# Kernel optimization log

Measured on AMD Instinct MI355X. Metric: run time of the kernel, lower is better.

## Reference

```python
import jax, jax.numpy as jnp
import numpy as np

NUM_HEADS = 8
SCALE_BASE = 512.0
GN_EPS = 1e-5


def rotate_every_two(x):
    x1 = x[..., ::2]
    x2 = x[..., 1::2]
    return jnp.stack([-x2, x1], axis=-1).reshape(x.shape)


def xpos_apply(x, downscale):
    # x: [B, T, D]; XPOS rotary with length-dependent scale (offset=0)
    L, D = x.shape[1], x.shape[2]
    half = D // 2
    scale_vec = (jnp.arange(0, D, 2, dtype=jnp.float32) + 0.4 * D) / (1.4 * D)  # [half]
    pos = jnp.arange(L, dtype=jnp.float32)
    scale = scale_vec[None, :] ** (pos[:, None] / SCALE_BASE)  # [L, half]
    inv_freq = 1.0 / (10000.0 ** (jnp.arange(half, dtype=jnp.float32) / half))
    sinusoid = pos[:, None] * inv_freq[None, :]  # [L, half]
    sin, cos = jnp.sin(sinusoid), jnp.cos(sinusoid)
    if downscale:
        scale = 1.0 / scale
    sin_s = jnp.repeat(sin * scale, 2, axis=-1)  # duplicate_interleave -> [L, D]
    cos_s = jnp.repeat(cos * scale, 2, axis=-1)
    return x * cos_s + rotate_every_two(x) * sin_s


def decay_mask_fn(T, num_heads):
    # gamma per head; decay stored as log(gamma) so mask = gamma^(i-j) on lower triangle
    s, e = np.log(1.0 / 32.0), np.log(1.0 / 512.0)
    gamma = 1.0 - jnp.exp(jnp.linspace(s, e, num_heads).astype(jnp.float32))
    log_decay = jnp.log(gamma)  # [H], negative
    idx = jnp.arange(T)
    expo = (idx[:, None] - idx[None, :]).astype(jnp.float32)  # i - j
    tri = (idx[:, None] >= idx[None, :])
    expo_safe = jnp.where(tri, expo, 0.0)
    mask = jnp.exp(log_decay[:, None, None] * expo_safe) * tri  # [H, T, T]
    scale = jnp.sqrt(mask.sum(axis=-1, keepdims=True))  # [H, T, 1]
    return mask / scale


def setup_inputs() -> dict:
    key = jax.random.key(0)
    ks = jax.random.split(key, 4)
    B, T, E = 2, 2048, 1024
    V = 2 * E
    return {
        "hidden_states": jax.random.normal(ks[0], (B, T, E), dtype=jnp.float32),
        "w_qkv": jax.random.normal(ks[1], (E, 2 * E + V), dtype=jnp.float32) * 0.02,
        "b_qkv": jnp.zeros((2 * E + V,), dtype=jnp.float32),
        "w_g": jax.random.normal(ks[2], (E, V), dtype=jnp.float32) * 0.02,
        "b_g": jnp.zeros((V,), dtype=jnp.float32),
        "w_p": jax.random.normal(ks[3], (V, E), dtype=jnp.float32) * 0.02,
        "b_p": jnp.zeros((E,), dtype=jnp.float32),
    }


def reference(hidden_states, w_qkv, b_qkv, w_g, b_g, w_p, b_p):
    B, T, E = hidden_states.shape
    H = NUM_HEADS
    V = 2 * E
    dk, dv = E // H, V // H

    qkv = hidden_states @ w_qkv + b_qkv
    q, k, v = qkv[..., :E], qkv[..., E:2 * E], qkv[..., 2 * E:]
    q = xpos_apply(q, downscale=False)
    k = xpos_apply(k, downscale=True)

    # split heads -> [B, H, T, d]
    q = q.reshape(B, T, H, dk).transpose(0, 2, 1, 3)
    k = k.reshape(B, T, H, dk).transpose(0, 2, 1, 3)
    v = v.reshape(B, T, H, dv).transpose(0, 2, 1, 3)

    mask = decay_mask_fn(T, H)  # [H, T, T]

    # parallel retention
    retention = jnp.einsum("bhid,bhjd->bhij", q, k) * (dk ** -0.5)
    retention = retention * mask[None]  # [B, H, T, T]
    out = jnp.einsum("bhij,bhjv->bhiv", retention, v)

    # current_kv = sum_j mask[h, -1, j] * k_j (x) v_j
    curr_kv = jnp.einsum("hj,bhjk,bhjv->bhkv", mask[:, -1, :], k, v)

    retention_out = out.transpose(0, 2, 1, 3).reshape(B, T, V)

    # GroupNorm(num_groups=H, affine=False) over v_dim channels
    g = retention_out.reshape(B * T, H, dv)
    mu = g.mean(axis=-1, keepdims=True)
    var = ((g - mu) ** 2).mean(axis=-1, keepdims=True)
    normed = ((g - mu) / jnp.sqrt(var + GN_EPS)).reshape(B, T, V)

    gated = jax.nn.silu(hidden_states @ w_g + b_g) * normed
    proj = gated @ w_p + b_p
    return proj, curr_kv
```

## Files before the change

### kernel.cpp

```cpp
#include <hip/hip_runtime.h>
#include <math.h>

#define BT      4096
#define T_SEQ   2048
#define E_DIM   1024
#define V_DIM   2048
#define DK      128
#define DV      256
#define QKV_LD  4096

typedef unsigned short ushort_t;
typedef __attribute__((ext_vector_type(8)))  short bf16x8;
typedef __attribute__((ext_vector_type(4)))  unsigned short u16x4;
typedef __attribute__((ext_vector_type(16))) float f32x16;

__device__ __forceinline__ void decay_params(int h, float& ld, float& gamma) {
    const float s0 = -3.4657359027997265f;
    const float e0 = -6.2383246250395092f;
    float lin = s0 + (e0 - s0) * ((float)h * (1.0f / 7.0f));
    gamma = 1.0f - expf(lin);
    ld = logf(gamma);
}

__device__ __forceinline__ short f2bf(float f) {
    unsigned u = __float_as_uint(f);
    unsigned r = (u + 0x7fffu + ((u >> 16) & 1u)) >> 16;
    return (short)r;
}
__device__ __forceinline__ float bf2f(ushort_t u) {
    return __uint_as_float((unsigned)u << 16);
}

__device__ __forceinline__ void async_copy16(void* lds, const void* g) {
    __builtin_amdgcn_global_load_lds(
        (const __attribute__((address_space(1))) unsigned int*)g,
        (__attribute__((address_space(3))) unsigned int*)lds, 16, 0, 0);
}

__global__ __launch_bounds__(256)
void f32_to_bf16_kernel(const float* __restrict__ in, ushort_t* __restrict__ out)
{
    int i = (blockIdx.x * 256 + threadIdx.x) * 8;
    float4 a = *(const float4*)&in[i];
    float4 b = *(const float4*)&in[i + 4];
    bf16x8 o;
    o[0] = f2bf(a.x); o[1] = f2bf(a.y); o[2] = f2bf(a.z); o[3] = f2bf(a.w);
    o[4] = f2bf(b.x); o[5] = f2bf(b.y); o[6] = f2bf(b.z); o[7] = f2bf(b.w);
    *(bf16x8*)&out[i] = o;
}

__global__ __launch_bounds__(256)
void transpose_w_kernel(const float* __restrict__ W, ushort_t* __restrict__ Wt,
                        int K, int N)
{
    __shared__ float tile[32][33];
    const int k0 = blockIdx.y * 32, n0 = blockIdx.x * 32;
    const int t = threadIdx.x;
    const int r = t >> 3, c = (t & 7) * 4;
    float4 v = *(const float4*)&W[(size_t)(k0 + r) * N + n0 + c];
    tile[r][c] = v.x; tile[r][c + 1] = v.y; tile[r][c + 2] = v.z; tile[r][c + 3] = v.w;
    __syncthreads();
    u16x4 o;
    o[0] = (ushort_t)f2bf(tile[c][r]);
    o[1] = (ushort_t)f2bf(tile[c + 1][r]);
    o[2] = (ushort_t)f2bf(tile[c + 2][r]);
    o[3] = (ushort_t)f2bf(tile[c + 3][r]);
    *(u16x4*)&Wt[(size_t)(n0 + r) * K + k0 + c] = o;
}

__global__ __launch_bounds__(512, 2)
void gemm256p8(const ushort_t* __restrict__ A,
               const ushort_t* __restrict__ Bt,
               const float* __restrict__ bias,
               float* __restrict__ C, int ldc, int nkt)
{
    __shared__ ushort_t As[2 * 16384];
    __shared__ ushort_t Bs[2 * 16384];

    const int tid = threadIdx.x;
    const int wid = tid >> 6, l = tid & 63;
    const int lc = l & 31, q = l >> 5;
    const int wr = wid >> 2, wc = wid & 3;
    const int m0 = blockIdx.y * 256, n0 = blockIdx.x * 256;

    const int sra = tid >> 3;
    const int spa = (tid & 7) ^ (sra & 7);
    const ushort_t* gA = A + (size_t)(m0 + sra) * 1024 + spa * 8;
    const int srb = tid >> 2;
    const int spb = (tid & 3) ^ ((srb >> 1) & 3);
    const ushort_t* gB = Bt + (size_t)(n0 + srb) * 1024 + spb * 8;
    const int da = tid * 8;

    int arow0 = (wr * 128 +  0 + lc) * 64;
    int arow1 = (wr * 128 + 32 + lc) * 64;
    int arow2 = (wr * 128 + 64 + lc) * 64;
    int arow3 = (wr * 128 + 96 + lc) * 64;
    int sk0 = ((0 * 2 + q) ^ (lc & 7)) * 8;
    int sk1 = ((1 * 2 + q) ^ (lc & 7)) * 8;
    int sk2 = ((2 * 2 + q) ^ (lc & 7)) * 8;
    int sk3 = ((3 * 2 + q) ^ (lc & 7)) * 8;
    int brow0 = (wc * 64 +  0 + lc) * 32;
    int brow1 = (wc * 64 + 32 + lc) * 32;
    int tk0 = ((0 + q) ^ ((lc >> 1) & 3)) * 8;
    int tk1 = ((2 + q) ^ ((lc >> 1) & 3)) * 8;
    int tk2 = 8192 + ((0 + q) ^ ((lc >> 1) & 3)) * 8;
    int tk3 = 8192 + ((2 + q) ^ ((lc >> 1) & 3)) * 8;

    f32x16 acc[4][2];
    #pragma unroll
    for (int mi = 0; mi < 4; ++mi)
        #pragma unroll
        for (int ni = 0; ni < 2; ++ni)
            #pragma unroll
            for (int e = 0; e < 16; ++e) acc[mi][ni][e] = 0.0f;

    async_copy16(&As[da],          gA);
    async_copy16(&As[8192 + da],   gA + 131072);
    async_copy16(&Bs[da],          gB);
    async_copy16(&Bs[4096 + da],   gB + 131072);
    async_copy16(&As[4096 + da],   gA + 65536);
    async_copy16(&As[12288 + da],  gA + 196608);
    async_copy16(&Bs[8192 + da],   gB + 32);
    async_copy16(&Bs[12288 + da],  gB + 131072 + 32);
    gA += 64; gB += 64;
    asm volatile("s_waitcnt vmcnt(0)" ::: "memory");
    __builtin_amdgcn_s_barrier();

    int cur = 0;
    for (int t = 0; t < nkt - 1; ++t) {
        const int cb = cur * 16384;
        const int nb = 16384 - cb;
        bf16x8 a00 = *(const bf16x8*)&As[cb + arow0 + sk0];
        bf16x8 a01 = *(const bf16x8*)&As[cb + arow0 + sk1];
        bf16x8 a10 = *(const bf16x8*)&As[cb + arow1 + sk0];
        bf16x8 a11 = *(const bf16x8*)&As[cb + arow1 + sk1];
        bf16x8 b00 = *(const bf16x8*)&Bs[cb + brow0 + tk0];
        bf16x8 b01 = *(const bf16x8*)&Bs[cb + brow0 + tk1];
        bf16x8 b10 = *(const bf16x8*)&Bs[cb + brow1 + tk0];
        bf16x8 b11 = *(const bf16x8*)&Bs[cb + brow1 + tk1];
        async_copy16(&As[nb + da],        gA);
        async_copy16(&As[nb + 8192 + da], gA + 131072);
        async_copy16(&Bs[nb + da],        gB);
        async_copy16(&Bs[nb + 4096 + da], gB + 131072);
        __builtin_amdgcn_s_barrier();
        asm volatile("s_waitcnt lgkmcnt(0)" ::: "memory");
        __builtin_amdgcn_s_setprio(1);
        acc[0][0] = __builtin_amdgcn_mfma_f32_32x32x16_bf16(a00, b00, acc[0][0], 0, 0, 0);
        acc[0][1] = __builtin_amdgcn_mfma_f32_32x32x16_bf16(a00, b10, acc[0][1], 0, 0, 0);
        acc[1][0] = __builtin_amdgcn_mfma_f32_32x32x16_bf16(a10, b00, acc[1][0], 0, 0, 0);
        acc[1][1] = __builtin_amdgcn_mfma_f32_32x32x16_bf16(a10, b10, acc[1][1], 0, 0, 0);
        acc[0][0] = __builtin_amdgcn_mfma_f32_32x32x16_bf16(a01, b01, acc[0][0], 0, 0, 0);
        acc[0][1] = __builtin_amdgcn_mfma_f32_32x32x16_bf16(a01, b11, acc[0][1], 0, 0, 0);
        acc[1][0] = __builtin_amdgcn_mfma_f32_32x32x16_bf16(a11, b01, acc[1][0], 0, 0, 0);
        acc[1][1] = __builtin_amdgcn_mfma_f32_32x32x16_bf16(a11, b11, acc[1][1], 0, 0, 0);
        __builtin_amdgcn_s_setprio(0);
        asm volatile("s_waitcnt vmcnt(6)" ::: "memory");
        __builtin_amdgcn_s_barrier();
        bf16x8 a20 = *(const bf16x8*)&As[cb + arow2 + sk0];
        bf16x8 a21 = *(const bf16x8*)&As[cb + arow2 + sk1];
        bf16x8 a30 = *(const bf16x8*)&As[cb + arow3 + sk0];
        bf16x8 a31 = *(const bf16x8*)&As[cb + arow3 + sk1];
        async_copy16(&As[nb + 4096 + da],  gA + 65536);
        async_copy16(&As[nb + 12288 + da], gA + 196608);
        __builtin_amdgcn_s_barrier();
        asm volatile("s_waitcnt lgkmcnt(0)" ::: "memory");
        __builtin_amdgcn_s_setprio(1);
        acc[2][0] = __builtin_amdgcn_mfma_f32_32x32x16_bf16(a20, b00, acc[2][0], 0, 0, 0);
        acc[2][1] = __builtin_amdgcn_mfma_f32_32x32x16_bf16(a20, b10, acc[2][1], 0, 0, 0);
        acc[3][0] = __builtin_amdgcn_mfma_f32_32x32x16_bf16(a30, b00, acc[3][0], 0, 0, 0);
        acc[3][1] = __builtin_amdgcn_mfma_f32_32x32x16_bf16(a30, b10, acc[3][1], 0, 0, 0);
        acc[2][0] = __builtin_amdgcn_mfma_f32_32x32x16_bf16(a21, b01, acc[2][0], 0, 0, 0);
        acc[2][1] = __builtin_amdgcn_mfma_f32_32x32x16_bf16(a21, b11, acc[2][1], 0, 0, 0);
        acc[3][0] = __builtin_amdgcn_mfma_f32_32x32x16_bf16(a31, b01, acc[3][0], 0, 0, 0);
        acc[3][1] = __builtin_amdgcn_mfma_f32_32x32x16_bf16(a31, b11, acc[3][1], 0, 0, 0);
        __builtin_amdgcn_s_setprio(0);
        asm volatile("s_waitcnt vmcnt(6)" ::: "memory");
        __builtin_amdgcn_s_barrier();
        bf16x8 a02 = *(const bf16x8*)&As[cb + arow0 + sk2];
        bf16x8 a03 = *(const bf16x8*)&As[cb + arow0 + sk3];
        bf16x8 a12 = *(const bf16x8*)&As[cb + arow1 + sk2];
        bf16x8 a13 = *(const bf16x8*)&As[cb + arow1 + sk3];
        bf16x8 b02 = *(const bf16x8*)&Bs[cb + brow0 + tk2];
        bf16x8 b03 = *(const bf16x8*)&Bs[cb + brow0 + tk3];
        bf16x8 b12 = *(const bf16x8*)&Bs[cb + brow1 + tk2];
        bf16x8 b13 = *(const bf16x8*)&Bs[cb + brow1 + tk3];
        async_copy16(&Bs[nb + 8192 + da],  gB + 32);
        async_copy16(&Bs[nb + 12288 + da], gB + 131072 + 32);
        gA += 64; gB += 64;
        __builtin_amdgcn_s_barrier();
        asm volatile("s_waitcnt lgkmcnt(0)" ::: "memory");
        __builtin_amdgcn_s_setprio(1);
        acc[0][0] = __builtin_amdgcn_mfma_f32_32x32x16_bf16(a02, b02, acc[0][0], 0, 0, 0);
        acc[0][1] = __builtin_amdgcn_mfma_f32_32x32x16_bf16(a02, b12, acc[0][1], 0, 0, 0);
        acc[1][0] = __builtin_amdgcn_mfma_f32_32x32x16_bf16(a12, b02, acc[1][0], 0, 0, 0);
        acc[1][1] = __builtin_amdgcn_mfma_f32_32x32x16_bf16(a12, b12, acc[1][1], 0, 0, 0);
        acc[0][0] = __builtin_amdgcn_mfma_f32_32x32x16_bf16(a03, b03, acc[0][0], 0, 0, 0);
        acc[0][1] = __builtin_amdgcn_mfma_f32_32x32x16_bf16(a03, b13, acc[0][1], 0, 0, 0);
        acc[1][0] = __builtin_amdgcn_mfma_f32_32x32x16_bf16(a13, b03, acc[1][0], 0, 0, 0);
        acc[1][1] = __builtin_amdgcn_mfma_f32_32x32x16_bf16(a13, b13, acc[1][1], 0, 0, 0);
        __builtin_amdgcn_s_setprio(0);
        __builtin_amdgcn_s_barrier();
        bf16x8 a22 = *(const bf16x8*)&As[cb + arow2 + sk2];
        bf16x8 a23 = *(const bf16x8*)&As[cb + arow2 + sk3];
        bf16x8 a32 = *(const bf16x8*)&As[cb + arow3 + sk2];
        bf16x8 a33 = *(const bf16x8*)&As[cb + arow3 + sk3];
        __builtin_amdgcn_s_barrier();
        asm volatile("s_waitcnt lgkmcnt(0)" ::: "memory");
        __builtin_amdgcn_s_setprio(1);
        acc[2][0] = __builtin_amdgcn_mfma_f32_32x32x16_bf16(a22, b02, acc[2][0], 0, 0, 0);
        acc[2][1] = __builtin_amdgcn_mfma_f32_32x32x16_bf16(a22, b12, acc[2][1], 0, 0, 0);
        acc[3][0] = __builtin_amdgcn_mfma_f32_32x32x16_bf16(a32, b02, acc[3][0], 0, 0, 0);
        acc[3][1] = __builtin_amdgcn_mfma_f32_32x32x16_bf16(a32, b12, acc[3][1], 0, 0, 0);
        acc[2][0] = __builtin_amdgcn_mfma_f32_32x32x16_bf16(a23, b03, acc[2][0], 0, 0, 0);
        acc[2][1] = __builtin_amdgcn_mfma_f32_32x32x16_bf16(a23, b13, acc[2][1], 0, 0, 0);
        acc[3][0] = __builtin_amdgcn_mfma_f32_32x32x16_bf16(a33, b03, acc[3][0], 0, 0, 0);
        acc[3][1] = __builtin_amdgcn_mfma_f32_32x32x16_bf16(a33, b13, acc[3][1], 0, 0, 0);
        __builtin_amdgcn_s_setprio(0);
        asm volatile("s_waitcnt vmcnt(4)" ::: "memory");
        __builtin_amdgcn_s_barrier();
        cur ^= 1;
    }

    {
        const int cb = cur * 16384;
        bf16x8 a00 = *(const bf16x8*)&As[cb + arow0 + sk0];
        bf16x8 a01 = *(const bf16x8*)&As[cb + arow0 + sk1];
        bf16x8 a10 = *(const bf16x8*)&As[cb + arow1 + sk0];
        bf16x8 a11 = *(const bf16x8*)&As[cb + arow1 + sk1];
        bf16x8 b00 = *(const bf16x8*)&Bs[cb + brow0 + tk0];
        bf16x8 b01 = *(const bf16x8*)&Bs[cb + brow0 + tk1];
        bf16x8 b10 = *(const bf16x8*)&Bs[cb + brow1 + tk0];
        bf16x8 b11 = *(const bf16x8*)&Bs[cb + brow1 + tk1];
        __builtin_amdgcn_s_barrier();
        asm volatile("s_waitcnt lgkmcnt(0)" ::: "memory");
        __builtin_amdgcn_s_setprio(1);
        acc[0][0] = __builtin_amdgcn_mfma_f32_32x32x16_bf16(a00, b00, acc[0][0], 0, 0, 0);
        acc[0][1] = __builtin_amdgcn_mfma_f32_32x32x16_bf16(a00, b10, acc[0][1], 0, 0, 0);
        acc[1][0] = __builtin_amdgcn_mfma_f32_32x32x16_bf16(a10, b00, acc[1][0], 0, 0, 0);
        acc[1][1] = __builtin_amdgcn_mfma_f32_32x32x16_bf16(a10, b10, acc[1][1], 0, 0, 0);
        acc[0][0] = __builtin_amdgcn_mfma_f32_32x32x16_bf16(a01, b01, acc[0][0], 0, 0, 0);
        acc[0][1] = __builtin_amdgcn_mfma_f32_32x32x16_bf16(a01, b11, acc[0][1], 0, 0, 0);
        acc[1][0] = __builtin_amdgcn_mfma_f32_32x32x16_bf16(a11, b01, acc[1][0], 0, 0, 0);
        acc[1][1] = __builtin_amdgcn_mfma_f32_32x32x16_bf16(a11, b11, acc[1][1], 0, 0, 0);
        __builtin_amdgcn_s_setprio(0);
        asm volatile("s_waitcnt vmcnt(2)" ::: "memory");
        __builtin_amdgcn_s_barrier();
        bf16x8 a20 = *(const bf16x8*)&As[cb + arow2 + sk0];
        bf16x8 a21 = *(const bf16x8*)&As[cb + arow2 + sk1];
        bf16x8 a30 = *(const bf16x8*)&As[cb + arow3 + sk0];
        bf16x8 a31 = *(const bf16x8*)&As[cb + arow3 + sk1];
        __builtin_amdgcn_s_barrier();
        asm volatile("s_waitcnt lgkmcnt(0)" ::: "memory");
        __builtin_amdgcn_s_setprio(1);
        acc[2][0] = __builtin_amdgcn_mfma_f32_32x32x16_bf16(a20, b00, acc[2][0], 0, 0, 0);
        acc[2][1] = __builtin_amdgcn_mfma_f32_32x32x16_bf16(a20, b10, acc[2][1], 0, 0, 0);
        acc[3][0] = __builtin_amdgcn_mfma_f32_32x32x16_bf16(a30, b00, acc[3][0], 0, 0, 0);
        acc[3][1] = __builtin_amdgcn_mfma_f32_32x32x16_bf16(a30, b10, acc[3][1], 0, 0, 0);
        acc[2][0] = __builtin_amdgcn_mfma_f32_32x32x16_bf16(a21, b01, acc[2][0], 0, 0, 0);
        acc[2][1] = __builtin_amdgcn_mfma_f32_32x32x16_bf16(a21, b11, acc[2][1], 0, 0, 0);
        acc[3][0] = __builtin_amdgcn_mfma_f32_32x32x16_bf16(a31, b01, acc[3][0], 0, 0, 0);
        acc[3][1] = __builtin_amdgcn_mfma_f32_32x32x16_bf16(a31, b11, acc[3][1], 0, 0, 0);
        __builtin_amdgcn_s_setprio(0);
        asm volatile("s_waitcnt vmcnt(0)" ::: "memory");
        __builtin_amdgcn_s_barrier();
        bf16x8 a02 = *(const bf16x8*)&As[cb + arow0 + sk2];
        bf16x8 a03 = *(const bf16x8*)&As[cb + arow0 + sk3];
        bf16x8 a12 = *(const bf16x8*)&As[cb + arow1 + sk2];
        bf16x8 a13 = *(const bf16x8*)&As[cb + arow1 + sk3];
        bf16x8 b02 = *(const bf16x8*)&Bs[cb + brow0 + tk2];
        bf16x8 b03 = *(const bf16x8*)&Bs[cb + brow0 + tk3];
        bf16x8 b12 = *(const bf16x8*)&Bs[cb + brow1 + tk2];
        bf16x8 b13 = *(const bf16x8*)&Bs[cb + brow1 + tk3];
        __builtin_amdgcn_s_barrier();
        asm volatile("s_waitcnt lgkmcnt(0)" ::: "memory");
        __builtin_amdgcn_s_setprio(1);
        acc[0][0] = __builtin_amdgcn_mfma_f32_32x32x16_bf16(a02, b02, acc[0][0], 0, 0, 0);
        acc[0][1] = __builtin_amdgcn_mfma_f32_32x32x16_bf16(a02, b12, acc[0][1], 0, 0, 0);
        acc[1][0] = __builtin_amdgcn_mfma_f32_32x32x16_bf16(a12, b02, acc[1][0], 0, 0, 0);
        acc[1][1] = __builtin_amdgcn_mfma_f32_32x32x16_bf16(a12, b12, acc[1][1], 0, 0, 0);
        acc[0][0] = __builtin_amdgcn_mfma_f32_32x32x16_bf16(a03, b03, acc[0][0], 0, 0, 0);
        acc[0][1] = __builtin_amdgcn_mfma_f32_32x32x16_bf16(a03, b13, acc[0][1], 0, 0, 0);
        acc[1][0] = __builtin_amdgcn_mfma_f32_32x32x16_bf16(a13, b03, acc[1][0], 0, 0, 0);
        acc[1][1] = __builtin_amdgcn_mfma_f32_32x32x16_bf16(a13, b13, acc[1][1], 0, 0, 0);
        __builtin_amdgcn_s_setprio(0);
        __builtin_amdgcn_s_barrier();
        bf16x8 a22 = *(const bf16x8*)&As[cb + arow2 + sk2];
        bf16x8 a23 = *(const bf16x8*)&As[cb + arow2 + sk3];
        bf16x8 a32 = *(const bf16x8*)&As[cb + arow3 + sk2];
        bf16x8 a33 = *(const bf16x8*)&As[cb + arow3 + sk3];
        asm volatile("s_waitcnt lgkmcnt(0)" ::: "memory");
        __builtin_amdgcn_s_setprio(1);
        acc[2][0] = __builtin_amdgcn_mfma_f32_32x32x16_bf16(a22, b02, acc[2][0], 0, 0, 0);
        acc[2][1] = __builtin_amdgcn_mfma_f32_32x32x16_bf16(a22, b12, acc[2][1], 0, 0, 0);
        acc[3][0] = __builtin_amdgcn_mfma_f32_32x32x16_bf16(a32, b02, acc[3][0], 0, 0, 0);
        acc[3][1] = __builtin_amdgcn_mfma_f32_32x32x16_bf16(a32, b12, acc[3][1], 0, 0, 0);
        acc[2][0] = __builtin_amdgcn_mfma_f32_32x32x16_bf16(a23, b03, acc[2][0], 0, 0, 0);
        acc[2][1] = __builtin_amdgcn_mfma_f32_32x32x16_bf16(a23, b13, acc[2][1], 0, 0, 0);
        acc[3][0] = __builtin_amdgcn_mfma_f32_32x32x16_bf16(a33, b03, acc[3][0], 0, 0, 0);
        acc[3][1] = __builtin_amdgcn_mfma_f32_32x32x16_bf16(a33, b13, acc[3][1], 0, 0, 0);
        __builtin_amdgcn_s_setprio(0);
    }

    #pragma unroll
    for (int ni = 0; ni < 2; ++ni) {
        const int col = n0 + wc * 64 + ni * 32 + lc;
        const float bb = bias[col];
        #pragma unroll
        for (int mi = 0; mi < 4; ++mi) {
            #pragma unroll
            for (int r = 0; r < 16; ++r) {
                const int row = m0 + wr * 128 + mi * 32 + (r & 3) + 8 * (r >> 2) + 4 * q;
                C[(size_t)row * ldc + col] = acc[mi][ni][r] + bb;
            }
        }
    }
}

template<int EPI>
__global__ __launch_bounds__(256)
void gemm_bf16(const ushort_t* __restrict__ A, int lda,
               const ushort_t* __restrict__ Bt, int ldb,
               const float* __restrict__ bias,
               void* __restrict__ Cv, int ldc,
               const void* __restrict__ extra, int lde,
               int nkt)
{
    __shared__ ushort_t As[3 * 128 * 32];
    __shared__ ushort_t Bs[3 * 128 * 32];

    const int tid = threadIdx.x;
    const int w  = tid >> 6, l = tid & 63;
    const int lc = l & 31, q = l >> 5;
    const int wr = w >> 1, wc = w & 1;
    const int m0 = blockIdx.y * 128, n0 = blockIdx.x * 128;

    const int r0 = tid >> 2,         kc0 = (tid & 3) ^ ((r0 >> 1) & 3);
    const int r1 = (256 + tid) >> 2, kc1 = (tid & 3) ^ ((r1 >> 1) & 3);
    const ushort_t* gA0 = A  + (size_t)(m0 + r0) * lda + kc0 * 8;
    const ushort_t* gA1 = A  + (size_t)(m0 + r1) * lda + kc1 * 8;
    const ushort_t* gB0 = Bt + (size_t)(n0 + r0) * ldb + kc0 * 8;
    const ushort_t* gB1 = Bt + (size_t)(n0 + r1) * ldb + kc1 * 8;
    const int s0 = w * 512;
    const int s1 = 2048 + w * 512;

    const int sl = (lc >> 1) & 3;
    int aoff[2][2], boff[2][2];
    #pragma unroll
    for (int mi = 0; mi < 2; ++mi)
        #pragma unroll
        for (int ks = 0; ks < 2; ++ks) {
            const int kk = ks * 2 + q;
            aoff[mi][ks] = ((wr * 64 + mi * 32 + lc) * 4 + (kk ^ sl)) * 8;
            boff[mi][ks] = ((wc * 64 + mi * 32 + lc) * 4 + (kk ^ sl)) * 8;
        }

    f32x16 acc[2][2];
    #pragma unroll
    for (int mi = 0; mi < 2; ++mi)
        #pragma unroll
        for (int ni = 0; ni < 2; ++ni)
            #pragma unroll
            for (int e = 0; e < 16; ++e) acc[mi][ni][e] = 0.0f;

    auto stage = [&](int bb) {
        async_copy16(&As[bb + s0], gA0); async_copy16(&As[bb + s1], gA1);
        async_copy16(&Bs[bb + s0], gB0); async_copy16(&Bs[bb + s1], gB1);
        gA0 += 32; gA1 += 32; gB0 += 32; gB1 += 32;
    };
    auto compute = [&](int cb) {
        bf16x8 a[2][2], b[2][2];
        #pragma unroll
        for (int mi = 0; mi < 2; ++mi)
            #pragma unroll
            for (int ks = 0; ks < 2; ++ks) {
                a[mi][ks] = *(const bf16x8*)&As[cb + aoff[mi][ks]];
                b[mi][ks] = *(const bf16x8*)&Bs[cb + boff[mi][ks]];
            }
        #pragma unroll
        for (int ks = 0; ks < 2; ++ks)
            #pragma unroll
            for (int mi = 0; mi < 2; ++mi)
                #pragma unroll
                for (int ni = 0; ni < 2; ++ni)
                    acc[mi][ni] = __builtin_amdgcn_mfma_f32_32x32x16_bf16(
                        a[mi][ks], b[ni][ks], acc[mi][ni], 0, 0, 0);
    };

    stage(0); stage(4096);
    int bs = 8192;
    int bc = 0;
    for (int kt = 0; kt < nkt - 2; ++kt) {
        asm volatile("s_waitcnt vmcnt(4)" ::: "memory");
        __builtin_amdgcn_s_barrier();
        stage(bs);
        compute(bc);
        bs = bc;
        bc = (bc == 8192) ? 0 : bc + 4096;
    }
    asm volatile("s_waitcnt vmcnt(4)" ::: "memory");
    __builtin_amdgcn_s_barrier();
    compute(bc);
    bc = (bc == 8192) ? 0 : bc + 4096;
    asm volatile("s_waitcnt vmcnt(0)" ::: "memory");
    __builtin_amdgcn_s_barrier();
    compute(bc);

    #pragma unroll
    for (int ni = 0; ni < 2; ++ni) {
        const int col = n0 + wc * 64 + ni * 32 + lc;
        const float bb = bias[col];
        #pragma unroll
        for (int mi = 0; mi < 2; ++mi) {
            #pragma unroll
            for (int r = 0; r < 16; ++r) {
                const int row = m0 + wr * 64 + mi * 32 + (r & 3) + 8 * (r >> 2) + 4 * q;
                float val = acc[mi][ni][r] + bb;
                if (EPI == 0) {
                    ((float*)Cv)[(size_t)row * ldc + col] = val;
                } else {
                    const float e = bf2f(((const ushort_t*)extra)[(size_t)row * lde + col]);
                    val = val / (1.0f + expf(-val)) * e;
                    ((ushort_t*)Cv)[(size_t)row * ldc + col] = (ushort_t)f2bf(val);
                }
            }
        }
    }
}

__global__ __launch_bounds__(256)
void gemm_tm64(const ushort_t* __restrict__ A, int lda,
               const ushort_t* __restrict__ Bt, int ldb,
               const float* __restrict__ bias,
               float* __restrict__ C, int ldc, int nkt)
{
    __shared__ ushort_t As[3 * 64 * 32];
    __shared__ ushort_t Bs[3 * 128 * 32];

    const int tid = threadIdx.x;
    const int w  = tid >> 6, l = tid & 63;
    const int lc = l & 31, q = l >> 5;
    const int wr = w >> 1, wc = w & 1;
    const int m0 = blockIdx.y * 64, n0 = blockIdx.x * 128;

    const int rA = tid >> 2,          kcA = (tid & 3) ^ ((rA >> 1) & 3);
    const int rB1 = (256 + tid) >> 2, kcB1 = (tid & 3) ^ ((rB1 >> 1) & 3);
    const ushort_t* gA  = A  + (size_t)(m0 + rA)  * lda + kcA  * 8;
    const ushort_t* gB0 = Bt + (size_t)(n0 + rA)  * ldb + kcA  * 8;
    const ushort_t* gB1 = Bt + (size_t)(n0 + rB1) * ldb + kcB1 * 8;
    const int sA  = w * 512;
    const int sB0 = w * 512;
    const int sB1 = 2048 + w * 512;

    const int sl = (lc >> 1) & 3;
    int aoff[2], boff[2][2];
    #pragma unroll
    for (int ks = 0; ks < 2; ++ks) {
        const int kk = ks * 2 + q;
        const int mrow = wr * 32 + lc;
        aoff[ks] = (mrow * 4 + (kk ^ sl)) * 8;
        #pragma unroll
        for (int ni = 0; ni < 2; ++ni) {
            const int nrow = wc * 64 + ni * 32 + lc;
            boff[ni][ks] = (nrow * 4 + (kk ^ sl)) * 8;
        }
    }

    f32x16 acc[2];
    #pragma unroll
    for (int ni = 0; ni < 2; ++ni)
        #pragma unroll
        for (int e = 0; e < 16; ++e) acc[ni][e] = 0.0f;

    auto stage = [&](int ab, int bb) {
        async_copy16(&As[ab + sA], gA);
        async_copy16(&Bs[bb + sB0], gB0); async_copy16(&Bs[bb + sB1], gB1);
        gA += 32; gB0 += 32; gB1 += 32;
    };
    auto compute = [&](int ab, int bb) {
        bf16x8 a[2], b[2][2];
        #pragma unroll
        for (int ks = 0; ks < 2; ++ks) {
            a[ks] = *(const bf16x8*)&As[ab + aoff[ks]];
            b[0][ks] = *(const bf16x8*)&Bs[bb + boff[0][ks]];
            b[1][ks] = *(const bf16x8*)&Bs[bb + boff[1][ks]];
        }
        #pragma unroll
        for (int ks = 0; ks < 2; ++ks)
            #pragma unroll
            for (int ni = 0; ni < 2; ++ni)
                acc[ni] = __builtin_amdgcn_mfma_f32_32x32x16_bf16(
                    a[ks], b[ni][ks], acc[ni], 0, 0, 0);
    };

    stage(0, 0); stage(2048, 4096);
    int as_ = 4096, bs_ = 8192;
    int ac_ = 0,    bc_ = 0;
    for (int kt = 0; kt < nkt - 2; ++kt) {
        asm volatile("s_waitcnt vmcnt(3)" ::: "memory");
        __builtin_amdgcn_s_barrier();
        stage(as_, bs_);
        compute(ac_, bc_);
        as_ = ac_; bs_ = bc_;
        ac_ = (ac_ == 4096) ? 0 : ac_ + 2048;
        bc_ = (bc_ == 8192) ? 0 : bc_ + 4096;
    }
    asm volatile("s_waitcnt vmcnt(3)" ::: "memory");
    __builtin_amdgcn_s_barrier();
    compute(ac_, bc_);
    ac_ = (ac_ == 4096) ? 0 : ac_ + 2048;
    bc_ = (bc_ == 8192) ? 0 : bc_ + 4096;
    asm volatile("s_waitcnt vmcnt(0)" ::: "memory");
    __builtin_amdgcn_s_barrier();
    compute(ac_, bc_);

    #pragma unroll
    for (int ni = 0; ni < 2; ++ni) {
        const int col = n0 + wc * 64 + ni * 32 + lc;
        const float bb = bias[col];
        #pragma unroll
        for (int r = 0; r < 16; ++r) {
            const int row = m0 + wr * 32 + (r & 3) + 8 * (r >> 2) + 4 * q;
            C[(size_t)row * ldc + col] = acc[ni][r] + bb;
        }
    }
}

__global__ __launch_bounds__(256)
void qk_prep(const float* __restrict__ qkv,
             ushort_t* __restrict__ qh, ushort_t* __restrict__ kh)
{
    const int row = blockIdx.x;
    const int t = threadIdx.x;
    const int b = row >> 11, trow = row & (T_SEQ - 1);
    const bool isK = t >= 128;
    const int col0 = (t & 127) * 8;
    const int h = col0 >> 7, d = col0 & 127;

    float ld, gamma;
    decay_params(h, ld, gamma);
    const float gsc = __expf(isK ? -ld * (float)(trow & 63) : ld * (float)(trow & 63));

    const float* src = qkv + (size_t)row * QKV_LD + (isK ? E_DIM : 0) + col0;
    float4 x0 = *(const float4*)src;
    float4 x1 = *(const float4*)(src + 4);
    float xv[8] = {x0.x, x0.y, x0.z, x0.w, x1.x, x1.y, x1.z, x1.w};

    const float tf = (float)trow * (1.0f / 512.0f);
    bf16x8 o;
    #pragma unroll
    for (int pi = 0; pi < 4; ++pi) {
        const int ip = col0 / 2 + pi;
        float sv = (2.0f * (float)ip + 409.6f) * (1.0f / 1433.6f);
        float e = __logf(sv) * tf;
        if (isK) e = -e;
        float sc = __expf(e);
        float invf = __expf((float)ip * -0.017988946038999563f);
        float sn, cs;
        sincosf((float)trow * invf, &sn, &cs);
        float c = cs * sc * gsc, s = sn * sc * gsc;
        float a = xv[2 * pi], bb = xv[2 * pi + 1];
        o[2 * pi]     = f2bf(a * c - bb * s);
        o[2 * pi + 1] = f2bf(bb * c + a * s);
    }
    ushort_t* dst = (isK ? kh : qh) + ((size_t)(b * 8 + h) * T_SEQ + trow) * 128 + d;
    *(bf16x8*)dst = o;
}

__global__ __launch_bounds__(256)
void v_transpose(const float* __restrict__ qkv, ushort_t* __restrict__ vt)
{
    __shared__ float tile[32][33];
    const int j0 = blockIdx.x * 32;
    const int zz = blockIdx.y;
    const int bh = zz >> 3, v0 = (zz & 7) * 32;
    const int b = bh >> 3, h = bh & 7;
    const int t = threadIdx.x;
    const int r = t >> 3, c = (t & 7) * 4;

    float4 x = *(const float4*)(qkv + (size_t)(b * T_SEQ + j0 + r) * QKV_LD
                                + 2 * E_DIM + h * DV + v0 + c);
    tile[r][c] = x.x; tile[r][c+1] = x.y; tile[r][c+2] = x.z; tile[r][c+3] = x.w;
    __syncthreads();
    u16x4 o;
    o[0] = (ushort_t)f2bf(tile[c][r]);
    o[1] = (ushort_t)f2bf(tile[c + 1][r]);
    o[2] = (ushort_t)f2bf(tile[c + 2][r]);
    o[3] = (ushort_t)f2bf(tile[c + 3][r]);
    *(u16x4*)&vt[((size_t)bh * 256 + v0 + r) * T_SEQ + j0 + c] = o;
}

__global__ __launch_bounds__(256)
void kt2_kernel(const ushort_t* __restrict__ kh, ushort_t* __restrict__ kt2)
{
    __shared__ ushort_t tile[32][40];
    const int j0 = blockIdx.x * 32;
    const int zz = blockIdx.y;
    const int bh = zz >> 2, k0 = (zz & 3) * 32;
    const int t = threadIdx.x;
    const int r = t >> 3, c = (t & 7) * 4;
    float ld, gamma; decay_params(bh & 7, ld, gamma);
    const float g63 = expf(ld * 63.0f);
    *(u16x4*)&tile[r][c] = *(const u16x4*)&kh[((size_t)bh * T_SEQ + j0 + r) * 128 + k0 + c];
    __syncthreads();
    u16x4 o;
    o[0] = (ushort_t)f2bf(bf2f(tile[c][r])     * g63);
    o[1] = (ushort_t)f2bf(bf2f(tile[c + 1][r]) * g63);
    o[2] = (ushort_t)f2bf(bf2f(tile[c + 2][r]) * g63);
    o[3] = (ushort_t)f2bf(bf2f(tile[c + 3][r]) * g63);
    *(u16x4*)&kt2[((size_t)bh * 128 + k0 + r) * T_SEQ + j0 + c] = o;
}

__global__ __launch_bounds__(256)
void chunk_kv(const ushort_t* __restrict__ vt, const ushort_t* __restrict__ kt2,
              ushort_t* __restrict__ Abuf)
{
    const int c = blockIdx.x;
    const int bh = blockIdx.y;
    const int tid = threadIdx.x;
    const int w = tid >> 6, l = tid & 63, lc = l & 31, q = l >> 5;
    const int j0 = c * 64;

    f32x16 acc[2][4];
    #pragma unroll
    for (int mi = 0; mi < 2; ++mi)
        #pragma unroll
        for (int ni = 0; ni < 4; ++ni)
            #pragma unroll
            for (int e = 0; e < 16; ++e) acc[mi][ni][e] = 0.0f;

    #pragma unroll
    for (int ks = 0; ks < 4; ++ks) {
        bf16x8 a[2], bfr[4];
        #pragma unroll
        for (int mi = 0; mi < 2; ++mi)
            a[mi] = *(const bf16x8*)(vt + ((size_t)bh * 256 + w * 64 + mi * 32 + lc) * T_SEQ
                                     + j0 + ks * 16 + q * 8);
        #pragma unroll
        for (int ni = 0; ni < 4; ++ni)
            bfr[ni] = *(const bf16x8*)(kt2 + ((size_t)bh * 128 + ni * 32 + lc) * T_SEQ
                                       + j0 + ks * 16 + q * 8);
        #pragma unroll
        for (int mi = 0; mi < 2; ++mi)
            #pragma unroll
            for (int ni = 0; ni < 4; ++ni)
                acc[mi][ni] = __builtin_amdgcn_mfma_f32_32x32x16_bf16(
                    a[mi], bfr[ni], acc[mi][ni], 0, 0, 0);
    }

    ushort_t* ab = Abuf + (size_t)(bh * 32 + c) * 256 * 128;
    #pragma unroll
    for (int mi = 0; mi < 2; ++mi)
        #pragma unroll
        for (int ni = 0; ni < 4; ++ni)
            #pragma unroll
            for (int r = 0; r < 16; ++r) {
                const int v = w * 64 + mi * 32 + (r & 3) + 8 * (r >> 2) + 4 * q;
                const int k = ni * 32 + lc;
                ab[(size_t)v * 128 + k] = (ushort_t)f2bf(acc[mi][ni][r]);
            }
}

__global__ __launch_bounds__(256)
void scan_state(const ushort_t* __restrict__ Abuf, ushort_t* __restrict__ St,
                float* __restrict__ ckv)
{
    const int blk = blockIdx.x;
    const int bh = blk >> 7, sub = blk & 127;
    const int tid = threadIdx.x;
    const int v = sub * 2 + (tid >> 7), k = tid & 127;

    float ld, gamma;
    decay_params(bh & 7, ld, gamma);
    const float g64 = expf(ld * 64.0f);

    const size_t base = ((size_t)bh * 32 * 256 + v) * 128 + k;
    const size_t cstr = 256 * 128;
    float s = 0.0f;
    for (int c = 0; c < 32; ++c) {
        const size_t off = base + (size_t)c * cstr;
        St[off] = (ushort_t)f2bf(gamma * s);
        s = g64 * s + bf2f(Abuf[off]);
    }
    const float inv_scale = rsqrtf((1.0f - expf(ld * (float)T_SEQ)) / (1.0f - gamma));
    ckv[((size_t)bh * 128 + k) * 256 + v] = s * inv_scale;
}

__global__ __launch_bounds__(64)
void retention_chunk(const ushort_t* __restrict__ qh,
                     const ushort_t* __restrict__ kh,
                     const ushort_t* __restrict__ vt,
                     const ushort_t* __restrict__ St,
                     ushort_t* __restrict__ normed)
{
    const int it = blockIdx.x;
    const int bh = blockIdx.y;
    const int b = bh >> 3, h = bh & 7;
    const int c = it >> 1, w = it & 1;
    const int l = threadIdx.x, lc = l & 31, q = l >> 5;
    const int i0 = it * 32;
    const size_t bhT = (size_t)bh * T_SEQ;

    float ld, gamma;
    decay_params(h, ld, gamma);

    bf16x8 qf[8];
    {
        const ushort_t* qp = qh + (bhT + i0 + lc) * 128 + q * 8;
        #pragma unroll
        for (int c8 = 0; c8 < 8; ++c8)
            qf[c8] = *(const bf16x8*)(qp + c8 * 16);
    }

    f32x16 acc[8];
    #pragma unroll
    for (int vg = 0; vg < 8; ++vg)
        #pragma unroll
        for (int e = 0; e < 16; ++e) acc[vg][e] = 0.0f;

    if (c > 0) {
        const ushort_t* sp = St + ((size_t)(bh * 32 + c) * 256 + lc) * 128 + q * 8;
        #pragma unroll
        for (int vg = 0; vg < 8; ++vg) {
            const ushort_t* spv = sp + (size_t)vg * 32 * 128;
            #pragma unroll
            for (int ks = 0; ks < 8; ++ks) {
                bf16x8 sb = *(const bf16x8*)(spv + ks * 16);
                acc[vg] = __builtin_amdgcn_mfma_f32_32x32x16_bf16(
                    qf[ks], sb, acc[vg], 0, 0, 0);
            }
        }
    }

    for (int jt2 = 0; jt2 <= w; ++jt2) {
        const int j0 = c * 64 + jt2 * 32;

        f32x16 s;
        #pragma unroll
        for (int e = 0; e < 16; ++e) s[e] = 0.0f;
        const ushort_t* kp = kh + (bhT + j0 + lc) * 128 + q * 8;
        #pragma unroll
        for (int c8 = 0; c8 < 8; ++c8) {
            bf16x8 ka = *(const bf16x8*)(kp + c8 * 16);
            s = __builtin_amdgcn_mfma_f32_32x32x16_bf16(ka, qf[c8], s, 0, 0, 0);
        }

        float sv[16];
        #pragma unroll
        for (int r = 0; r < 16; ++r) {
            float val = s[r];
            if (jt2 == w) {
                int jr_ = (r & 3) + 8 * (r >> 2) + 4 * q;
                val = (jr_ <= lc) ? val : 0.0f;
            }
            sv[r] = val;
        }

        bf16x8 pa0, pa1;
        #pragma unroll
        for (int e = 0; e < 4; ++e) {
            float t1 = __shfl_xor(sv[e + 4], 32);
            float t0 = __shfl_xor(sv[e], 32);
            pa0[e]     = f2bf(q ? t1 : sv[e]);
            pa0[e + 4] = f2bf(q ? sv[e + 4] : t0);
            float t3 = __shfl_xor(sv[e + 12], 32);
            float t2 = __shfl_xor(sv[e + 8], 32);
            pa1[e]     = f2bf(q ? t3 : sv[e + 8]);
            pa1[e + 4] = f2bf(q ? sv[e + 12] : t2);
        }

        #pragma unroll
        for (int vg = 0; vg < 8; ++vg) {
            const ushort_t* vp = vt + ((size_t)bh * 256 + vg * 32 + lc) * T_SEQ + j0 + q * 8;
            bf16x8 vb0 = *(const bf16x8*)vp;
            bf16x8 vb1 = *(const bf16x8*)(vp + 16);
            acc[vg] = __builtin_amdgcn_mfma_f32_32x32x16_bf16(pa0, vb0, acc[vg], 0, 0, 0);
            acc[vg] = __builtin_amdgcn_mfma_f32_32x32x16_bf16(pa1, vb1, acc[vg], 0, 0, 0);
        }
    }

    #pragma unroll
    for (int r = 0; r < 16; ++r) {
        const int il = (r & 3) + 8 * (r >> 2) + 4 * q;
        const int i  = i0 + il;
        float denom = (1.0f - expf(ld * (float)(i + 1))) / (1.0f - gamma);
        float fs = 0.08838834764831845f * rsqrtf(denom);
        float vals[8];
        float a1 = 0.0f, a2 = 0.0f;
        #pragma unroll
        for (int vg = 0; vg < 8; ++vg) {
            float x = acc[vg][r] * fs;
            vals[vg] = x;
            a1 += x; a2 += x * x;
        }
        a1 += __shfl_xor(a1, 1);  a2 += __shfl_xor(a2, 1);
        a1 += __shfl_xor(a1, 2);  a2 += __shfl_xor(a2, 2);
        a1 += __shfl_xor(a1, 4);  a2 += __shfl_xor(a2, 4);
        a1 += __shfl_xor(a1, 8);  a2 += __shfl_xor(a2, 8);
        a1 += __shfl_xor(a1, 16); a2 += __shfl_xor(a2, 16);
        float mu = a1 * (1.0f / 256.0f);
        float var = a2 * (1.0f / 256.0f) - mu * mu;
        float rs = rsqrtf(var + 1e-5f);
        ushort_t* op = normed + ((size_t)(b * T_SEQ + i)) * V_DIM + h * DV + lc;
        #pragma unroll
        for (int vg = 0; vg < 8; ++vg)
            op[vg * 32] = (ushort_t)f2bf((vals[vg] - mu) * rs);
    }
}

extern "C" void kernel_launch(void* const* d_in, const int* in_sizes, int n_in,
                              void* d_out, int out_size, void* d_ws, size_t ws_size,
                              hipStream_t stream)
{
    const float* hs    = (const float*)d_in[0];
    const float* w_qkv = (const float*)d_in[1];
    const float* b_qkv = (const float*)d_in[2];
    const float* w_g   = (const float*)d_in[3];
    const float* b_g   = (const float*)d_in[4];
    const float* w_p   = (const float*)d_in[5];
    const float* b_p   = (const float*)d_in[6];
    float* out = (float*)d_out;

    const size_t MB = 1024 * 1024;
    float*    qkv      = (float*)d_ws;
    ushort_t* Abuf     = (ushort_t*)d_ws;
    ushort_t* normed   = (ushort_t*)d_ws;
    ushort_t* Stbuf    = (ushort_t*)((char*)d_ws + 32 * MB);
    ushort_t* gated_bf = (ushort_t*)((char*)d_ws + 32 * MB);
    ushort_t* wg_t     = (ushort_t*)((char*)d_ws + 56 * MB);
    ushort_t* wp_t     = (ushort_t*)((char*)d_ws + 60 * MB);
    ushort_t* qh       = (ushort_t*)((char*)d_ws + 64 * MB);
    ushort_t* vt       = (ushort_t*)((char*)d_ws + 72 * MB);
    ushort_t* wqkv_t   = (ushort_t*)((char*)d_ws + 88 * MB);
    ushort_t* kh       = (ushort_t*)((char*)d_ws + 88 * MB);
    ushort_t* hs_bf    = (ushort_t*)d_out;
    ushort_t* kt2      = (ushort_t*)((char*)d_out + 8 * MB);
    float*    ckv_out  = out + (size_t)BT * E_DIM;

    f32_to_bf16_kernel<<<dim3(2048), 256, 0, stream>>>(hs, hs_bf);
    transpose_w_kernel<<<dim3(128, 32), 256, 0, stream>>>(w_qkv, wqkv_t, E_DIM, 4096);

    gemm256p8<<<dim3(16, 16), 512, 0, stream>>>(
        hs_bf, wqkv_t, b_qkv, qkv, QKV_LD, E_DIM / 64);

    qk_prep<<<dim3(BT), 256, 0, stream>>>(qkv, qh, kh);
    v_transpose<<<dim3(64, 128), 256, 0, stream>>>(qkv, vt);
    kt2_kernel<<<dim3(64, 64), 256, 0, stream>>>(kh, kt2);

    chunk_kv<<<dim3(32, 16), 256, 0, stream>>>(vt, kt2, Abuf);
    scan_state<<<dim3(2048), 256, 0, stream>>>(Abuf, Stbuf, ckv_out);
    retention_chunk<<<dim3(64, 16), 64, 0, stream>>>(qh, kh, vt, Stbuf, normed);

    transpose_w_kernel<<<dim3(64, 32), 256, 0, stream>>>(w_g, wg_t, E_DIM, V_DIM);
    transpose_w_kernel<<<dim3(32, 64), 256, 0, stream>>>(w_p, wp_t, V_DIM, E_DIM);

    gemm_bf16<1><<<dim3(16, 32), 256, 0, stream>>>(
        hs_bf, E_DIM, wg_t, E_DIM, b_g, gated_bf, V_DIM, normed, V_DIM, E_DIM / 32);

    gemm_tm64<<<dim3(8, 64), 256, 0, stream>>>(
        gated_bf, V_DIM, wp_t, V_DIM, b_p, out, E_DIM, V_DIM / 32);
}
```

Measured before the change: 303.2 us.

## Rewrite gate GEMM as 512-thread 128x256 tile kernel with split-phase pipelining

Replaces the templated 256-thread 128x128 gate GEMM with a dedicated 512-thread kernel that computes 128x256 tiles using a K-step of 64, double-buffered LDS and two half-steps per iteration. Async global loads for the next tile are interleaved with MFMA phases using barriers, waitcnt, and setprio. The aim is better operand reuse per block and better overlap of loads with matrix math. In exchange, the grid halves to 256 blocks, which may leave CUs underutilized, and the hardcoded leading dimensions make the kernel shape-specific.

```diff
diff --git a/kernel.cpp b/kernel.cpp
--- a/kernel.cpp
+++ b/kernel.cpp
@@ -316,43 +316,43 @@
     }
 }
 
-template<int EPI>
-__global__ __launch_bounds__(256)
-void gemm_bf16(const ushort_t* __restrict__ A, int lda,
-               const ushort_t* __restrict__ Bt, int ldb,
-               const float* __restrict__ bias,
-               void* __restrict__ Cv, int ldc,
-               const void* __restrict__ extra, int lde,
-               int nkt)
-{
-    __shared__ ushort_t As[3 * 128 * 32];
-    __shared__ ushort_t Bs[3 * 128 * 32];
+__global__ __launch_bounds__(512)
+void gemm_gate_p8(const ushort_t* __restrict__ A,
+                  const ushort_t* __restrict__ Bt,
+                  const float* __restrict__ bias,
+                  ushort_t* __restrict__ C, int ldc,
+                  const ushort_t* __restrict__ extra, int lde,
+                  int nkt)
+{
+    __shared__ ushort_t As[2 * 8192];
+    __shared__ ushort_t Bs[2 * 16384];
 
     const int tid = threadIdx.x;
-    const int w  = tid >> 6, l = tid & 63;
+    const int wid = tid >> 6, l = tid & 63;
     const int lc = l & 31, q = l >> 5;
-    const int wr = w >> 1, wc = w & 1;
-    const int m0 = blockIdx.y * 128, n0 = blockIdx.x * 128;
-
-    const int r0 = tid >> 2,         kc0 = (tid & 3) ^ ((r0 >> 1) & 3);
-    const int r1 = (256 + tid) >> 2, kc1 = (tid & 3) ^ ((r1 >> 1) & 3);
-    const ushort_t* gA0 = A  + (size_t)(m0 + r0) * lda + kc0 * 8;
-    const ushort_t* gA1 = A  + (size_t)(m0 + r1) * lda + kc1 * 8;
-    const ushort_t* gB0 = Bt + (size_t)(n0 + r0) * ldb + kc0 * 8;
-    const ushort_t* gB1 = Bt + (size_t)(n0 + r1) * ldb + kc1 * 8;
-    const int s0 = w * 512;
-    const int s1 = 2048 + w * 512;
-
-    const int sl = (lc >> 1) & 3;
-    int aoff[2][2], boff[2][2];
-    #pragma unroll
-    for (int mi = 0; mi < 2; ++mi)
-        #pragma unroll
-        for (int ks = 0; ks < 2; ++ks) {
-            const int kk = ks * 2 + q;
-            aoff[mi][ks] = ((wr * 64 + mi * 32 + lc) * 4 + (kk ^ sl)) * 8;
-            boff[mi][ks] = ((wc * 64 + mi * 32 + lc) * 4 + (kk ^ sl)) * 8;
-        }
+    const int wr = wid >> 2, wc = wid & 3;
+    const int m0 = blockIdx.y * 128, n0 = blockIdx.x * 256;
+
+    const int sra = tid >> 3;
+    const int spa = (tid & 7) ^ (sra & 7);
+    const ushort_t* gA = A + (size_t)(m0 + sra) * 1024 + spa * 8;
+    const int srb = tid >> 2;
+    const int spb = (tid & 3) ^ ((srb >> 1) & 3);
+    const ushort_t* gB = Bt + (size_t)(n0 + srb) * 1024 + spb * 8;
+    const int da = tid * 8;
+
+    int arow0 = (wr * 64 +  0 + lc) * 64;
+    int arow1 = (wr * 64 + 32 + lc) * 64;
+    int sk0 = ((0 * 2 + q) ^ (lc & 7)) * 8;
+    int sk1 = ((1 * 2 + q) ^ (lc & 7)) * 8;
+    int sk2 = ((2 * 2 + q) ^ (lc & 7)) * 8;
+    int sk3 = ((3 * 2 + q) ^ (lc & 7)) * 8;
+    int brow0 = (wc * 64 +  0 + lc) * 32;
+    int brow1 = (wc * 64 + 32 + lc) * 32;
+    int tk0 = ((0 + q) ^ ((lc >> 1) & 3)) * 8;
+    int tk1 = ((2 + q) ^ ((lc >> 1) & 3)) * 8;
+    int tk2 = 8192 + ((0 + q) ^ ((lc >> 1) & 3)) * 8;
+    int tk3 = 8192 + ((2 + q) ^ ((lc >> 1) & 3)) * 8;
 
     f32x16 acc[2][2];
     #pragma unroll
@@ -362,48 +362,119 @@
             #pragma unroll
             for (int e = 0; e < 16; ++e) acc[mi][ni][e] = 0.0f;
 
-    auto stage = [&](int bb) {
-        async_copy16(&As[bb + s0], gA0); async_copy16(&As[bb + s1], gA1);
-        async_copy16(&Bs[bb + s0], gB0); async_copy16(&Bs[bb + s1], gB1);
-        gA0 += 32; gA1 += 32; gB0 += 32; gB1 += 32;
-    };
-    auto compute = [&](int cb) {
-        bf16x8 a[2][2], b[2][2];
-        #pragma unroll
-        for (int mi = 0; mi < 2; ++mi)
-            #pragma unroll
-            for (int ks = 0; ks < 2; ++ks) {
-                a[mi][ks] = *(const bf16x8*)&As[cb + aoff[mi][ks]];
-                b[mi][ks] = *(const bf16x8*)&Bs[cb + boff[mi][ks]];
-            }
-        #pragma unroll
-        for (int ks = 0; ks < 2; ++ks)
-            #pragma unroll
-            for (int mi = 0; mi < 2; ++mi)
-                #pragma unroll
-                for (int ni = 0; ni < 2; ++ni)
-                    acc[mi][ni] = __builtin_amdgcn_mfma_f32_32x32x16_bf16(
-                        a[mi][ks], b[ni][ks], acc[mi][ni], 0, 0, 0);
-    };
-
-    stage(0); stage(4096);
-    int bs = 8192;
-    int bc = 0;
-    for (int kt = 0; kt < nkt - 2; ++kt) {
-        asm volatile("s_waitcnt vmcnt(4)" ::: "memory");
-        __builtin_amdgcn_s_barrier();
-        stage(bs);
-        compute(bc);
-        bs = bc;
-        bc = (bc == 8192) ? 0 : bc + 4096;
-    }
-    asm volatile("s_waitcnt vmcnt(4)" ::: "memory");
-    __builtin_amdgcn_s_barrier();
-    compute(bc);
-    bc = (bc == 8192) ? 0 : bc + 4096;
+    async_copy16(&As[da],          gA);
+    async_copy16(&As[4096 + da],   gA + 65536);
+    async_copy16(&Bs[da],          gB);
+    async_copy16(&Bs[4096 + da],   gB + 131072);
+    async_copy16(&Bs[8192 + da],   gB + 32);
+    async_copy16(&Bs[12288 + da],  gB + 131072 + 32);
+    gA += 64; gB += 64;
     asm volatile("s_waitcnt vmcnt(0)" ::: "memory");
     __builtin_amdgcn_s_barrier();
-    compute(bc);
+
+    int cur = 0;
+    for (int t = 0; t < nkt - 1; ++t) {
+        const int ca = cur * 8192,  na = 8192 - ca;
+        const int cb = cur * 16384, nb = 16384 - cb;
+        bf16x8 a00 = *(const bf16x8*)&As[ca + arow0 + sk0];
+        bf16x8 a01 = *(const bf16x8*)&As[ca + arow0 + sk1];
+        bf16x8 a10 = *(const bf16x8*)&As[ca + arow1 + sk0];
+        bf16x8 a11 = *(const bf16x8*)&As[ca + arow1 + sk1];
+        bf16x8 b00 = *(const bf16x8*)&Bs[cb + brow0 + tk0];
+        bf16x8 b01 = *(const bf16x8*)&Bs[cb + brow0 + tk1];
+        bf16x8 b10 = *(const bf16x8*)&Bs[cb + brow1 + tk0];
+        bf16x8 b11 = *(const bf16x8*)&Bs[cb + brow1 + tk1];
+        async_copy16(&As[na + da],        gA);
+        async_copy16(&As[na + 4096 + da], gA + 65536);
+        async_copy16(&Bs[nb + da],        gB);
+        async_copy16(&Bs[nb + 4096 + da], gB + 131072);
+        __builtin_amdgcn_s_barrier();
+        asm volatile("s_waitcnt lgkmcnt(0)" ::: "memory");
+        __builtin_amdgcn_s_setprio(1);
+        acc[0][0] = __builtin_amdgcn_mfma_f32_32x32x16_bf16(a00, b00, acc[0][0], 0, 0, 0);
+        acc[0][1] = __builtin_amdgcn_mfma_f32_32x32x16_bf16(a00, b10, acc[0][1], 0, 0, 0);
+        acc[1][0] = __builtin_amdgcn_mfma_f32_32x32x16_bf16(a10, b00, acc[1][0], 0, 0, 0);
+        acc[1][1] = __builtin_amdgcn_mfma_f32_32x32x16_bf16(a10, b10, acc[1][1], 0, 0, 0);
+        acc[0][0] = __builtin_amdgcn_mfma_f32_32x32x16_bf16(a01, b01, acc[0][0], 0, 0, 0);
+        acc[0][1] = __builtin_amdgcn_mfma_f32_32x32x16_bf16(a01, b11, acc[0][1], 0, 0, 0);
+        acc[1][0] = __builtin_amdgcn_mfma_f32_32x32x16_bf16(a11, b01, acc[1][0], 0, 0, 0);
+        acc[1][1] = __builtin_amdgcn_mfma_f32_32x32x16_bf16(a11, b11, acc[1][1], 0, 0, 0);
+        __builtin_amdgcn_s_setprio(0);
+        asm volatile("s_waitcnt vmcnt(4)" ::: "memory");
+        __builtin_amdgcn_s_barrier();
+        bf16x8 a02 = *(const bf16x8*)&As[ca + arow0 + sk2];
+        bf16x8 a03 = *(const bf16x8*)&As[ca + arow0 + sk3];
+        bf16x8 a12 = *(const bf16x8*)&As[ca + arow1 + sk2];
+        bf16x8 a13 = *(const bf16x8*)&As[ca + arow1 + sk3];
+        bf16x8 b02 = *(const bf16x8*)&Bs[cb + brow0 + tk2];
+        bf16x8 b03 = *(const bf16x8*)&Bs[cb + brow0 + tk3];
+        bf16x8 b12 = *(const bf16x8*)&Bs[cb + brow1 + tk2];
+        bf16x8 b13 = *(const bf16x8*)&Bs[cb + brow1 + tk3];
+        async_copy16(&Bs[nb + 8192 + da],  gB + 32);
+        async_copy16(&Bs[nb + 12288 + da], gB + 131072 + 32);
+        gA += 64; gB += 64;
+        __builtin_amdgcn_s_barrier();
+        asm volatile("s_waitcnt lgkmcnt(0)" ::: "memory");
+        __builtin_amdgcn_s_setprio(1);
+        acc[0][0] = __builtin_amdgcn_mfma_f32_32x32x16_bf16(a02, b02, acc[0][0], 0, 0, 0);
+        acc[0][1] = __builtin_amdgcn_mfma_f32_32x32x16_bf16(a02, b12, acc[0][1], 0, 0, 0);
+        acc[1][0] = __builtin_amdgcn_mfma_f32_32x32x16_bf16(a12, b02, acc[1][0], 0, 0, 0);
+        acc[1][1] = __builtin_amdgcn_mfma_f32_32x32x16_bf16(a12, b12, acc[1][1], 0, 0, 0);
+        acc[0][0] = __builtin_amdgcn_mfma_f32_32x32x16_bf16(a03, b03, acc[0][0], 0, 0, 0);
+        acc[0][1] = __builtin_amdgcn_mfma_f32_32x32x16_bf16(a03, b13, acc[0][1], 0, 0, 0);
+        acc[1][0] = __builtin_amdgcn_mfma_f32_32x32x16_bf16(a13, b03, acc[1][0], 0, 0, 0);
+        acc[1][1] = __builtin_amdgcn_mfma_f32_32x32x16_bf16(a13, b13, acc[1][1], 0, 0, 0);
+        __builtin_amdgcn_s_setprio(0);
+        asm volatile("s_waitcnt vmcnt(2)" ::: "memory");
+        __builtin_amdgcn_s_barrier();
+        cur ^= 1;
+    }
+
+    {
+        const int ca = cur * 8192;
+        const int cb = cur * 16384;
+        bf16x8 a00 = *(const bf16x8*)&As[ca + arow0 + sk0];
+        bf16x8 a01 = *(const bf16x8*)&As[ca + arow0 + sk1];
+        bf16x8 a10 = *(const bf16x8*)&As[ca + arow1 + sk0];
+        bf16x8 a11 = *(const bf16x8*)&As[ca + arow1 + sk1];
+        bf16x8 b00 = *(const bf16x8*)&Bs[cb + brow0 + tk0];
+        bf16x8 b01 = *(const bf16x8*)&Bs[cb + brow0 + tk1];
+        bf16x8 b10 = *(const bf16x8*)&Bs[cb + brow1 + tk0];
+        bf16x8 b11 = *(const bf16x8*)&Bs[cb + brow1 + tk1];
+        __builtin_amdgcn_s_barrier();
+        asm volatile("s_waitcnt lgkmcnt(0)" ::: "memory");
+        __builtin_amdgcn_s_setprio(1);
+        acc[0][0] = __builtin_amdgcn_mfma_f32_32x32x16_bf16(a00, b00, acc[0][0], 0, 0, 0);
+        acc[0][1] = __builtin_amdgcn_mfma_f32_32x32x16_bf16(a00, b10, acc[0][1], 0, 0, 0);
+        acc[1][0] = __builtin_amdgcn_mfma_f32_32x32x16_bf16(a10, b00, acc[1][0], 0, 0, 0);
+        acc[1][1] = __builtin_amdgcn_mfma_f32_32x32x16_bf16(a10, b10, acc[1][1], 0, 0, 0);
+        acc[0][0] = __builtin_amdgcn_mfma_f32_32x32x16_bf16(a01, b01, acc[0][0], 0, 0, 0);
+        acc[0][1] = __builtin_amdgcn_mfma_f32_32x32x16_bf16(a01, b11, acc[0][1], 0, 0, 0);
+        acc[1][0] = __builtin_amdgcn_mfma_f32_32x32x16_bf16(a11, b01, acc[1][0], 0, 0, 0);
+        acc[1][1] = __builtin_amdgcn_mfma_f32_32x32x16_bf16(a11, b11, acc[1][1], 0, 0, 0);
+        __builtin_amdgcn_s_setprio(0);
+        asm volatile("s_waitcnt vmcnt(0)" ::: "memory");
+        __builtin_amdgcn_s_barrier();
+        bf16x8 a02 = *(const bf16x8*)&As[ca + arow0 + sk2];
+        bf16x8 a03 = *(const bf16x8*)&As[ca + arow0 + sk3];
+        bf16x8 a12 = *(const bf16x8*)&As[ca + arow1 + sk2];
+        bf16x8 a13 = *(const bf16x8*)&As[ca + arow1 + sk3];
+        bf16x8 b02 = *(const bf16x8*)&Bs[cb + brow0 + tk2];
+        bf16x8 b03 = *(const bf16x8*)&Bs[cb + brow0 + tk3];
+        bf16x8 b12 = *(const bf16x8*)&Bs[cb + brow1 + tk2];
+        bf16x8 b13 = *(const bf16x8*)&Bs[cb + brow1 + tk3];
+        asm volatile("s_waitcnt lgkmcnt(0)" ::: "memory");
+        __builtin_amdgcn_s_setprio(1);
+        acc[0][0] = __builtin_amdgcn_mfma_f32_32x32x16_bf16(a02, b02, acc[0][0], 0, 0, 0);
+        acc[0][1] = __builtin_amdgcn_mfma_f32_32x32x16_bf16(a02, b12, acc[0][1], 0, 0, 0);
+        acc[1][0] = __builtin_amdgcn_mfma_f32_32x32x16_bf16(a12, b02, acc[1][0], 0, 0, 0);
+        acc[1][1] = __builtin_amdgcn_mfma_f32_32x32x16_bf16(a12, b12, acc[1][1], 0, 0, 0);
+        acc[0][0] = __builtin_amdgcn_mfma_f32_32x32x16_bf16(a03, b03, acc[0][0], 0, 0, 0);
+        acc[0][1] = __builtin_amdgcn_mfma_f32_32x32x16_bf16(a03, b13, acc[0][1], 0, 0, 0);
+        acc[1][0] = __builtin_amdgcn_mfma_f32_32x32x16_bf16(a13, b03, acc[1][0], 0, 0, 0);
+        acc[1][1] = __builtin_amdgcn_mfma_f32_32x32x16_bf16(a13, b13, acc[1][1], 0, 0, 0);
+        __builtin_amdgcn_s_setprio(0);
+    }
 
     #pragma unroll
     for (int ni = 0; ni < 2; ++ni) {
@@ -415,13 +486,9 @@
             for (int r = 0; r < 16; ++r) {
                 const int row = m0 + wr * 64 + mi * 32 + (r & 3) + 8 * (r >> 2) + 4 * q;
                 float val = acc[mi][ni][r] + bb;
-                if (EPI == 0) {
-                    ((float*)Cv)[(size_t)row * ldc + col] = val;
-                } else {
-                    const float e = bf2f(((const ushort_t*)extra)[(size_t)row * lde + col]);
-                    val = val / (1.0f + expf(-val)) * e;
-                    ((ushort_t*)Cv)[(size_t)row * ldc + col] = (ushort_t)f2bf(val);
-                }
+                const float e = bf2f(extra[(size_t)row * lde + col]);
+                val = val / (1.0f + expf(-val)) * e;
+                C[(size_t)row * ldc + col] = (ushort_t)f2bf(val);
             }
         }
     }
@@ -853,8 +920,8 @@
     transpose_w_kernel<<<dim3(64, 32), 256, 0, stream>>>(w_g, wg_t, E_DIM, V_DIM);
     transpose_w_kernel<<<dim3(32, 64), 256, 0, stream>>>(w_p, wp_t, V_DIM, E_DIM);
 
-    gemm_bf16<1><<<dim3(16, 32), 256, 0, stream>>>(
-        hs_bf, E_DIM, wg_t, E_DIM, b_g, gated_bf, V_DIM, normed, V_DIM, E_DIM / 32);
+    gemm_gate_p8<<<dim3(8, 32), 512, 0, stream>>>(
+        hs_bf, wg_t, b_g, gated_bf, V_DIM, normed, V_DIM, E_DIM / 64);
 
     gemm_tm64<<<dim3(8, 64), 256, 0, stream>>>(
         gated_bf, V_DIM, wp_t, V_DIM, b_p, out, E_DIM, V_DIM / 32);
```

Result: slower. 310.2 us (+2.3%).
